# Optimization experiments

Hardware: AMD Instinct MI355X
Metric: run time of the kernel (lower is better)

Reference implementation:

```python
import jax, jax.numpy as jnp
import numpy as np

H = 256          # hidden_size
ATOM_F = 133     # chemprop atom feature dim
BOND_F = 14      # chemprop bond feature dim
BOND_FDIM = ATOM_F + BOND_F  # chemprop concatenates source-atom + bond features
N = 400_000      # total atoms in batch
E = 800_000      # total directed bonds (pairs e, e^1)
N_MOLS = 13_000
DEPTH = 3


def setup_inputs() -> dict:
    key = jax.random.key(0)
    ks = jax.random.split(key, 16)
    f_atoms = jax.random.normal(ks[0], (N, ATOM_F), jnp.float32)
    f_bonds = jax.random.normal(ks[1], (E, BOND_FDIM), jnp.float32)
    # directed bonds stored in reverse-pairs: bond 2i is a->b, bond 2i+1 is b->a
    src0 = jax.random.randint(ks[2], (E // 2,), 0, N)
    dst0 = jax.random.randint(ks[3], (E // 2,), 0, N)
    src = jnp.stack([src0, dst0], axis=1).reshape(-1)
    dst = jnp.stack([dst0, src0], axis=1).reshape(-1)
    edge_index = jnp.stack([src, dst], axis=0).astype(jnp.int32)  # [2, E]
    rev_edge_index = (jnp.arange(E, dtype=jnp.int32) ^ 1)         # rev(e) = e^1
    atom_mol = jnp.sort(jax.random.randint(ks[4], (N,), 0, N_MOLS)).astype(jnp.int32)

    def glorot(k, shape):
        return (jax.random.normal(k, shape, jnp.float32) / np.float32(np.sqrt(shape[0])))

    W_i = glorot(ks[5], (BOND_FDIM, H))      # chemprop W_i (no bias)
    W_h = glorot(ks[6], (H, H))              # chemprop W_h (no bias)
    W_o = glorot(ks[7], (ATOM_F + H, H))     # chemprop W_o
    b_o = jnp.zeros((H,), jnp.float32)
    node_W = glorot(ks[8], (H, ATOM_F)); node_b = jnp.zeros((ATOM_F,), jnp.float32)
    edge_W = glorot(ks[9], (H, BOND_F)); edge_b = jnp.zeros((BOND_F,), jnp.float32)
    g_W1 = glorot(ks[10], (H, H)); g_b1 = jnp.zeros((H,), jnp.float32)
    g_W2 = glorot(ks[11], (H, 1)); g_b2 = jnp.zeros((1,), jnp.float32)
    return dict(f_atoms=f_atoms, f_bonds=f_bonds,
                W_i=W_i, W_h=W_h, W_o=W_o, b_o=b_o,
                node_W=node_W, node_b=node_b, edge_W=edge_W, edge_b=edge_b,
                g_W1=g_W1, g_b1=g_b1, g_W2=g_W2, g_b2=g_b2,
                edge_index=edge_index, rev_edge_index=rev_edge_index,
                atom_mol=atom_mol, n_mols=N_MOLS)


def reference(f_atoms, f_bonds, W_i, W_h, W_o, b_o,
              node_W, node_b, edge_W, edge_b,
              g_W1, g_b1, g_W2, g_b2,
              edge_index, rev_edge_index, atom_mol, n_mols):
    n_atoms = f_atoms.shape[0]
    src, dst = edge_index[0], edge_index[1]

    # --- chemprop D-MPNN encoder (bond messages, depth=3, dropout=0) ---
    inp = f_bonds @ W_i                   # [E, H]
    msg = jax.nn.relu(inp)
    for _ in range(DEPTH - 1):
        # sum of messages arriving at each atom
        a_msg = jax.ops.segment_sum(msg, dst, num_segments=n_atoms)   # [N, H]
        # message for bond e (src->dst): sum into src minus reverse message
        msg = jax.nn.relu(inp + (a_msg[src] - msg[rev_edge_index]) @ W_h)
    a_msg = jax.ops.segment_sum(msg, dst, num_segments=n_atoms)
    atom_hiddens = jax.nn.relu(jnp.concatenate([f_atoms, a_msg], axis=1) @ W_o + b_o)  # [N, H]

    # --- graph pooling: per-molecule SUM over a_scope (empty mols -> zeros) ---
    graph_emb = jax.ops.segment_sum(atom_hiddens, atom_mol, num_segments=n_mols)  # [M, H]

    # --- node head ---
    node_pred = atom_hiddens @ node_W + node_b                        # [N, ATOM_F]

    # --- edge head with reverse-bond dedup: keep e where e < rev(e) (even e) ---
    keep = jnp.arange(0, edge_index.shape[1], 2)
    bond_emb = 0.5 * (atom_hiddens[src[keep]] + atom_hiddens[dst[keep]])
    edge_pred = bond_emb @ edge_W + edge_b                            # [E/2, BOND_F]

    # --- graph head MLP ---
    graph_pred = jax.nn.relu(graph_emb @ g_W1 + g_b1) @ g_W2 + g_b2   # [M, 1]
    return node_pred, edge_pred, graph_pred
```

## Files before the change

### kernel.cpp

```cpp
#include <hip/hip_runtime.h>

#define NATOMS 400000
#define NEDGES 800000
#define NMOLS  13000
#define AF 133
#define BFdim 14
#define BFD 147

typedef __attribute__((ext_vector_type(8))) short  s16x8;
typedef __attribute__((ext_vector_type(8))) __bf16 b16x8;
typedef __attribute__((ext_vector_type(4))) float  f32x4;

__device__ __forceinline__ float bf2f(unsigned short u){
  union { unsigned int i; float f; } v; v.i = ((unsigned int)u) << 16; return v.f;
}
__device__ __forceinline__ unsigned short f2bf(float f){
  union { float ff; unsigned int i; } v; v.ff = f;
  unsigned int b = v.i + 0x7fffu + ((v.i >> 16) & 1u);
  return (unsigned short)(b >> 16);
}
__device__ __forceinline__ unsigned int pk2(float a, float b){
  unsigned int r;
  asm("v_cvt_pk_bf16_f32 %0, %1, %2" : "=v"(r) : "v"(a), "v"(b));
  return r;
}
__device__ __forceinline__ f32x4 mfma16(s16x8 a, s16x8 b, f32x4 c){
  return __builtin_amdgcn_mfma_f32_16x16x32_bf16(
      __builtin_bit_cast(b16x8, a), __builtin_bit_cast(b16x8, b), c, 0, 0, 0);
}
__device__ __forceinline__ void gload_lds16(const void* g, void* lds){
  __builtin_amdgcn_global_load_lds(
      (const __attribute__((address_space(1))) void*)g,
      (__attribute__((address_space(3))) void*)lds, 16, 0, 0);
}

__global__ void k_prep_weights(const float* __restrict__ W_i, const float* __restrict__ W_h,
                               const float* __restrict__ W_o, const float* __restrict__ node_W,
                               const float* __restrict__ edge_W,
                               ushort* __restrict__ Wif, ushort* __restrict__ Wof1,
                               ushort* __restrict__ Whf, ushort* __restrict__ Wof2,
                               ushort* __restrict__ nWf, ushort* __restrict__ eWf){
  int gid = blockIdx.x * 256 + threadIdx.x;
  ushort* dst; const float* src; int KB, Kv, Ns, idx;
  if      (gid <  40960){ idx = gid;          dst = Wif;  src = W_i;          KB = 5; Kv = 147; Ns = 256; }
  else if (gid <  81920){ idx = gid -  40960; dst = Wof1; src = W_o;          KB = 5; Kv = 133; Ns = 256; }
  else if (gid < 147456){ idx = gid -  81920; dst = Whf;  src = W_h;          KB = 8; Kv = 256; Ns = 256; }
  else if (gid < 212992){ idx = gid - 147456; dst = Wof2; src = W_o + 133*256;KB = 8; Kv = 256; Ns = 256; }
  else if (gid < 249856){ idx = gid - 212992; dst = nWf;  src = node_W;       KB = 8; Kv = 256; Ns = 133; }
  else if (gid < 253952){ idx = gid - 249856; dst = eWf;  src = edge_W;       KB = 8; Kv = 256; Ns = 14;  }
  else return;
  int j = idx & 7, lane = (idx >> 3) & 63, fi = idx >> 9;
  int kb = fi % KB, nb = fi / KB;
  int k = kb * 32 + ((lane >> 4) << 3) + j;
  int n = nb * 16 + (lane & 15);
  float v = 0.f;
  if (k < Kv && n < Ns) v = src[(size_t)k * Ns + n];
  dst[idx] = f2bf(v);
}

__global__ void k_hist(const int* __restrict__ key, int* __restrict__ deg){
  int e = blockIdx.x * 256 + threadIdx.x;
  if (e < NEDGES) atomicAdd(&deg[key[e]], 1);
}
__global__ void k_blocksum(const int* __restrict__ deg, int* __restrict__ bsum){
  __shared__ int s[256];
  int i = blockIdx.x * 256 + threadIdx.x;
  s[threadIdx.x] = (i < NATOMS) ? deg[i] : 0;
  __syncthreads();
  for (int st = 128; st > 0; st >>= 1){
    if (threadIdx.x < st) s[threadIdx.x] += s[threadIdx.x + st];
    __syncthreads();
  }
  if (threadIdx.x == 0) bsum[blockIdx.x] = s[0];
}
#define NBLK 1563
__global__ void k_scanblk(const int* __restrict__ bs, int* __restrict__ bo){
  __shared__ int s[2048];
  int t = threadIdx.x;
  s[2*t]   = (2*t   < NBLK) ? bs[2*t]   : 0;
  s[2*t+1] = (2*t+1 < NBLK) ? bs[2*t+1] : 0;
  int offset = 1;
  for (int d = 1024; d > 0; d >>= 1){
    __syncthreads();
    if (t < d){ int ai = offset*(2*t+1)-1, bi = offset*(2*t+2)-1; s[bi] += s[ai]; }
    offset <<= 1;
  }
  __syncthreads();
  if (t == 0) s[2047] = 0;
  for (int d = 1; d < 2048; d <<= 1){
    offset >>= 1;
    __syncthreads();
    if (t < d){ int ai = offset*(2*t+1)-1, bi = offset*(2*t+2)-1;
                int tmp = s[ai]; s[ai] = s[bi]; s[bi] += tmp; }
  }
  __syncthreads();
  if (2*t   < NBLK) bo[2*t]   = s[2*t];
  if (2*t+1 < NBLK) bo[2*t+1] = s[2*t+1];
}
__global__ void k_offs(const int* __restrict__ deg, const int* __restrict__ bo,
                       int* __restrict__ offs, int* __restrict__ cursor){
  __shared__ int s1[256], s2[256];
  int t = threadIdx.x;
  int i = blockIdx.x * 256 + t;
  int v = (i < NATOMS) ? deg[i] : 0;
  s1[t] = v;
  __syncthreads();
  int* rd = s1; int* wr = s2;
  for (int ofs = 1; ofs < 256; ofs <<= 1){
    wr[t] = rd[t] + ((t >= ofs) ? rd[t - ofs] : 0);
    __syncthreads();
    int* tmp = rd; rd = wr; wr = tmp;
  }
  if (i < NATOMS){
    int excl = rd[t] - v + bo[blockIdx.x];
    offs[i] = excl; cursor[i] = excl;
  }
  if (i == 0) offs[NATOMS] = NEDGES;
}
__global__ void k_fill(const int* __restrict__ key, int* __restrict__ cursor,
                       int* __restrict__ elist){
  int e = blockIdx.x * 256 + threadIdx.x;
  if (e < NEDGES){ int pos = atomicAdd(&cursor[key[e]], 1); elist[pos] = e; }
}
__global__ void k_pos(const int* __restrict__ elist, int* __restrict__ pos){
  int i = blockIdx.x * 256 + threadIdx.x;
  if (i < NEDGES) pos[elist[i]] = i;
}
__global__ void k_maps(const int* __restrict__ elist, const int* __restrict__ pos,
                       int* __restrict__ revp){
  int i = blockIdx.x * 256 + threadIdx.x;
  if (i < NEDGES) revp[i] = pos[elist[i] ^ 1];
}
__global__ void k_molstart(const int* __restrict__ atom_mol, int* __restrict__ molst){
  int m = blockIdx.x * 256 + threadIdx.x;
  if (m > NMOLS) return;
  int lo = 0, hi = NATOMS;
  while (lo < hi){ int mid = (lo + hi) >> 1; if (atom_mol[mid] < m) lo = mid + 1; else hi = mid; }
  molst[m] = lo;
}

__global__ __launch_bounds__(256) void k_fused_inpY(
    const float* __restrict__ FB, const ushort* __restrict__ Wif,
    const ushort* __restrict__ Whf, const int* __restrict__ pos,
    ushort* __restrict__ inp, ushort* __restrict__ Yout){
  __shared__ ushort At[64 * 256];
  const int t = threadIdx.x, w = t >> 6, l = t & 63;
  const long e0 = (long)blockIdx.x * 64;
  {
    int r = t >> 2, q = t & 3;
    #pragma unroll
    for (int c = 0; c < 4; c++){
      int col = 147 + q * 4 + c;
      if (col < 160){
        int byte = r * 384 + ((2 * col) ^ ((r & 7) << 4));
        *(ushort*)((char*)At + byte) = 0;
      }
    }
  }
  {
    const float4* src = (const float4*)(FB + e0 * 147);
    #pragma unroll
    for (int it = 0; it < 10; it++){
      int idx = t + it * 256;
      if (idx < 2352){
        float4 v = src[idx];
        int fi = idx * 4;
        #pragma unroll
        for (int j = 0; j < 4; j++){
          int f = fi + j;
          int row = (int)(((unsigned)f * 114131u) >> 24);
          int col = f - row * 147;
          int byte = row * 384 + ((2 * col) ^ ((row & 7) << 4));
          *(ushort*)((char*)At + byte) = f2bf((&v.x)[j]);
        }
      }
    }
  }
  __syncthreads();
  const int lr = l & 15, lg = l >> 4;
  f32x4 acc[4][4] = {};
  for (int kb = 0; kb < 5; kb++){
    s16x8 a[4], b[4];
    #pragma unroll
    for (int m = 0; m < 4; m++){
      int row = m * 16 + lr;
      int cb = (kb * 64 + (lg << 4)) ^ ((row & 7) << 4);
      a[m] = *(const s16x8*)((const char*)At + row * 384 + cb);
    }
    #pragma unroll
    for (int n = 0; n < 4; n++)
      b[n] = *(const s16x8*)(Wif + (size_t)(((w * 4 + n) * 5 + kb) * 64 + l) * 8);
    #pragma unroll
    for (int m = 0; m < 4; m++)
      #pragma unroll
      for (int n = 0; n < 4; n++)
        acc[m][n] = mfma16(a[m], b[n], acc[m][n]);
  }
  __syncthreads();
  #pragma unroll
  for (int m = 0; m < 4; m++){
    long pr[4];
    #pragma unroll
    for (int r = 0; r < 4; r++)
      pr[r] = (long)pos[e0 + m * 16 + lg * 4 + r] * 256;
    #pragma unroll
    for (int n = 0; n < 4; n++){
      int col = w * 64 + n * 16 + lr;
      #pragma unroll
      for (int r = 0; r < 4; r++){
        float v = acc[m][n][r];
        inp[pr[r] + col] = f2bf(v);
        int row = m * 16 + lg * 4 + r;
        int byte = row * 512 + ((2 * col) ^ ((row & 7) << 4));
        *(ushort*)((char*)At + byte) = f2bf(v > 0.f ? v : 0.f);
      }
    }
  }
  __syncthreads();
  f32x4 acc2[4][4] = {};
  for (int kb = 0; kb < 8; kb++){
    s16x8 a[4], b[4];
    #pragma unroll
    for (int m = 0; m < 4; m++){
      int row = m * 16 + lr;
      int cb = (kb * 64 + (lg << 4)) ^ ((row & 7) << 4);
      a[m] = *(const s16x8*)((const char*)At + row * 512 + cb);
    }
    #pragma unroll
    for (int n = 0; n < 4; n++)
      b[n] = *(const s16x8*)(Whf + (size_t)(((w * 4 + n) * 8 + kb) * 64 + l) * 8);
    #pragma unroll
    for (int m = 0; m < 4; m++)
      #pragma unroll
      for (int n = 0; n < 4; n++)
        acc2[m][n] = mfma16(a[m], b[n], acc2[m][n]);
  }
  #pragma unroll
  for (int m = 0; m < 4; m++){
    long dr[4];
    #pragma unroll
    for (int r = 0; r < 4; r++)
      dr[r] = (long)pos[e0 + ((m * 16 + lg * 4 + r) ^ 1)] * 256;
    #pragma unroll
    for (int n = 0; n < 4; n++){
      int col = w * 64 + n * 16 + lr;
      #pragma unroll
      for (int r = 0; r < 4; r++)
        Yout[dr[r] + col] = f2bf(acc2[m][n][r]);
    }
  }
}

__global__ __launch_bounds__(256) void k_Y(
    const ushort* __restrict__ A, const ushort* __restrict__ Whf,
    const int* __restrict__ revp, ushort* __restrict__ Yout){
  __shared__ ushort At[64 * 256];
  const int t = threadIdx.x, w = t >> 6, l = t & 63;
  const long e0 = (long)blockIdx.x * 64;
  const char* Ab = (const char*)(A + e0 * 256);
  #pragma unroll
  for (int i = 0; i < 8; i++){
    int dbase = (i * 4 + w) * 1024;
    int d = dbase + l * 16;
    int sw = ((d >> 9) & 7) << 4;
    gload_lds16(Ab + (d ^ sw), (char*)At + dbase);
  }
  __syncthreads();
  const int lr = l & 15, lg = l >> 4;
  f32x4 acc[4][4] = {};
  for (int kb = 0; kb < 8; kb++){
    s16x8 a[4], b[4];
    #pragma unroll
    for (int m = 0; m < 4; m++){
      int row = m * 16 + lr;
      int cb = (kb * 64 + (lg << 4)) ^ ((row & 7) << 4);
      a[m] = *(const s16x8*)((const char*)At + row * 512 + cb);
    }
    #pragma unroll
    for (int n = 0; n < 4; n++){
      int fi = (w * 4 + n) * 8 + kb;
      b[n] = *(const s16x8*)(Whf + (size_t)(fi * 64 + l) * 8);
    }
    #pragma unroll
    for (int m = 0; m < 4; m++)
      #pragma unroll
      for (int n = 0; n < 4; n++)
        acc[m][n] = mfma16(a[m], b[n], acc[m][n]);
  }
  #pragma unroll
  for (int m = 0; m < 4; m++){
    long dr[4];
    #pragma unroll
    for (int r = 0; r < 4; r++)
      dr[r] = (long)revp[e0 + m * 16 + lg * 4 + r] * 256;
    #pragma unroll
    for (int n = 0; n < 4; n++){
      int col = w * 64 + n * 16 + lr;
      #pragma unroll
      for (int r = 0; r < 4; r++)
        Yout[dr[r] + col] = f2bf(acc[m][n][r]);
    }
  }
}

template<bool SCATTER>
__global__ __launch_bounds__(256) void k_comb(
    const ushort* __restrict__ Yd, const ushort* __restrict__ inp,
    const int* __restrict__ revp, const int* __restrict__ offs,
    ushort* __restrict__ M){
  const int t = threadIdx.x, g = t >> 5, h = t & 31;
  const int a = blockIdx.x * 8 + g;
  const int beg = offs[a], end = offs[a + 1];
  const int deg = end - beg;
  if (deg == 0) return;
  if (deg <= 4){
    s16x8 y[4], vi[4];
    #pragma unroll
    for (int k = 0; k < 4; k++) if (k < deg){
      y[k]  = *(const s16x8*)(Yd  + (size_t)(beg + k) * 256 + h * 8);
      vi[k] = *(const s16x8*)(inp + (size_t)(beg + k) * 256 + h * 8);
    }
    float acc[8] = {};
    #pragma unroll
    for (int k = 0; k < 4; k++) if (k < deg){
      #pragma unroll
      for (int j = 0; j < 8; j++) acc[j] += bf2f((ushort)y[k][j]);
    }
    #pragma unroll
    for (int k = 0; k < 4; k++) if (k < deg){
      float vv[8];
      #pragma unroll
      for (int j = 0; j < 8; j++){
        float v = bf2f((ushort)vi[k][j]) + acc[j] - bf2f((ushort)y[k][j]);
        vv[j] = v > 0.f ? v : 0.f;
      }
      uint4 o;
      o.x = pk2(vv[0], vv[1]); o.y = pk2(vv[2], vv[3]);
      o.z = pk2(vv[4], vv[5]); o.w = pk2(vv[6], vv[7]);
      long wrow = SCATTER ? (long)revp[beg + k] : (long)(beg + k);
      *(uint4*)(M + wrow * 256 + h * 8) = o;
    }
  } else {
    float acc[8] = {};
    for (int i = beg; i < end; i++){
      s16x8 y = *(const s16x8*)(Yd + (size_t)i * 256 + h * 8);
      #pragma unroll
      for (int j = 0; j < 8; j++) acc[j] += bf2f((ushort)y[j]);
    }
    for (int i = beg; i < end; i++){
      s16x8 y  = *(const s16x8*)(Yd  + (size_t)i * 256 + h * 8);
      s16x8 vi = *(const s16x8*)(inp + (size_t)i * 256 + h * 8);
      float vv[8];
      #pragma unroll
      for (int j = 0; j < 8; j++){
        float v = bf2f((ushort)vi[j]) + acc[j] - bf2f((ushort)y[j]);
        vv[j] = v > 0.f ? v : 0.f;
      }
      uint4 o;
      o.x = pk2(vv[0], vv[1]); o.y = pk2(vv[2], vv[3]);
      o.z = pk2(vv[4], vv[5]); o.w = pk2(vv[6], vv[7]);
      long wrow = SCATTER ? (long)revp[i] : (long)i;
      *(uint4*)(M + wrow * 256 + h * 8) = o;
    }
  }
}

__global__ __launch_bounds__(256) void k_amsg_seq(
    const ushort* __restrict__ Md, const int* __restrict__ offs,
    ushort* __restrict__ amsg){
  const int t = threadIdx.x, g = t >> 5, h = t & 31;
  const int a = blockIdx.x * 8 + g;
  const int beg = offs[a], end = offs[a + 1];
  float acc[8] = {};
  for (int i = beg; i < end; i++){
    s16x8 v = *(const s16x8*)(Md + (size_t)i * 256 + h * 8);
    #pragma unroll
    for (int j = 0; j < 8; j++) acc[j] += bf2f((ushort)v[j]);
  }
  uint4 ov;
  ov.x = pk2(acc[0], acc[1]); ov.y = pk2(acc[2], acc[3]);
  ov.z = pk2(acc[4], acc[5]); ov.w = pk2(acc[6], acc[7]);
  *(uint4*)(amsg + (size_t)a * 256 + h * 8) = ov;
}

__global__ __launch_bounds__(256) void k_ah(
    const float* __restrict__ FA, const ushort* __restrict__ Wof1,
    const ushort* __restrict__ amsg, const ushort* __restrict__ Wof2,
    const float* __restrict__ b_o, ushort* __restrict__ ah){
  __shared__ ushort At[64 * 192];
  const int t = threadIdx.x, w = t >> 6, l = t & 63;
  const long r0 = (long)blockIdx.x * 64;
  {
    int r = t >> 2, q = t & 3;
    #pragma unroll
    for (int c = 0; c < 7; c++){
      int col = 133 + q * 7 + c;
      if (col < 160){
        int byte = r * 384 + ((2 * col) ^ ((r & 7) << 4));
        *(ushort*)((char*)At + byte) = 0;
      }
    }
  }
  {
    const float4* src = (const float4*)(FA + r0 * 133);
    #pragma unroll
    for (int it = 0; it < 9; it++){
      int idx = t + it * 256;
      if (idx < 2128){
        float4 v = src[idx];
        int fi = idx * 4;
        #pragma unroll
        for (int j = 0; j < 4; j++){
          int f = fi + j;
          int row = (int)(((unsigned)f * 126146u) >> 24);
          int col = f - row * 133;
          int byte = row * 384 + ((2 * col) ^ ((row & 7) << 4));
          *(ushort*)((char*)At + byte) = f2bf((&v.x)[j]);
        }
      }
    }
  }
  __syncthreads();
  const int lr = l & 15, lg = l >> 4;
  f32x4 acc[4][4] = {};
  for (int kb = 0; kb < 5; kb++){
    s16x8 a[4], b[4];
    #pragma unroll
    for (int m = 0; m < 4; m++){
      int row = m * 16 + lr;
      int cb = (kb * 64 + (lg << 4)) ^ ((row & 7) << 4);
      a[m] = *(const s16x8*)((const char*)At + row * 384 + cb);
    }
    #pragma unroll
    for (int n = 0; n < 4; n++)
      b[n] = *(const s16x8*)(Wof1 + (size_t)(((w * 4 + n) * 5 + kb) * 64 + l) * 8);
    #pragma unroll
    for (int m = 0; m < 4; m++)
      #pragma unroll
      for (int n = 0; n < 4; n++)
        acc[m][n] = mfma16(a[m], b[n], acc[m][n]);
  }
  for (int kb = 0; kb < 8; kb++){
    s16x8 a[4], b[4];
    #pragma unroll
    for (int m = 0; m < 4; m++)
      a[m] = *(const s16x8*)(amsg + (r0 + m * 16 + lr) * 256 + kb * 32 + lg * 8);
    #pragma unroll
    for (int n = 0; n < 4; n++)
      b[n] = *(const s16x8*)(Wof2 + (size_t)(((w * 4 + n) * 8 + kb) * 64 + l) * 8);
    #pragma unroll
    for (int m = 0; m < 4; m++)
      #pragma unroll
      for (int n = 0; n < 4; n++)
        acc[m][n] = mfma16(a[m], b[n], acc[m][n]);
  }
  #pragma unroll
  for (int m = 0; m < 4; m++){
    #pragma unroll
    for (int n = 0; n < 4; n++){
      int col = w * 64 + n * 16 + lr;
      float bo = b_o[col];
      long base = (r0 + m * 16 + lg * 4) * 256 + col;
      #pragma unroll
      for (int r = 0; r < 4; r++){
        float v = acc[m][n][r] + bo;
        ah[base + (long)r * 256] = f2bf(v > 0.f ? v : 0.f);
      }
    }
  }
}

__global__ __launch_bounds__(256) void k_nodeproj(
    const ushort* __restrict__ ah, const ushort* __restrict__ nWf,
    const ushort* __restrict__ eWf, const float* __restrict__ node_b,
    float* __restrict__ out_node, float* __restrict__ proj){
  const int t = threadIdx.x, w = t >> 6, l = t & 63, lr = l & 15, lg = l >> 4;
  const long r0 = (long)blockIdx.x * 64;
  f32x4 acc[4][3] = {};
  for (int kb = 0; kb < 8; kb++){
    s16x8 a[4];
    #pragma unroll
    for (int m = 0; m < 4; m++)
      a[m] = *(const s16x8*)(ah + (r0 + m * 16 + lr) * 256 + kb * 32 + lg * 8);
    s16x8 b[3];
    #pragma unroll
    for (int j = 0; j < 3; j++){
      int nt = w + 4 * j;
      int ntc = (nt <= 9) ? nt : 0;
      if (ntc == 9)
        b[j] = *(const s16x8*)(eWf + (size_t)(kb * 64 + l) * 8);
      else
        b[j] = *(const s16x8*)(nWf + (size_t)((ntc * 8 + kb) * 64 + l) * 8);
    }
    #pragma unroll
    for (int m = 0; m < 4; m++)
      #pragma unroll
      for (int j = 0; j < 3; j++)
        acc[m][j] = mfma16(a[m], b[j], acc[m][j]);
  }
  #pragma unroll
  for (int j = 0; j < 3; j++){
    int nt = w + 4 * j;
    if (nt > 9) continue;
    if (nt == 9){
      #pragma unroll
      for (int m = 0; m < 4; m++)
        #pragma unroll
        for (int r = 0; r < 4; r++)
          proj[(r0 + m * 16 + lg * 4 + r) * 16 + lr] = acc[m][j][r];
    } else {
      int col = nt * 16 + lr;
      if (col < AF){
        float nb = node_b[col];
        #pragma unroll
        for (int m = 0; m < 4; m++)
          #pragma unroll
          for (int r = 0; r < 4; r++)
            out_node[(r0 + m * 16 + lg * 4 + r) * AF + col] = acc[m][j][r] + nb;
      }
    }
  }
}

__global__ void k_edge_out(const int* __restrict__ edge_index, const float* __restrict__ proj,
                           const float* __restrict__ edge_b, float* __restrict__ out_edge){
  int gid = blockIdx.x * 256 + threadIdx.x;
  int i = gid >> 4, c = gid & 15;
  if (c < BFdim){
    int s = edge_index[2 * i];
    int d = edge_index[NEDGES + 2 * i];
    out_edge[(size_t)i * BFdim + c] =
        0.5f * (proj[(size_t)s * 16 + c] + proj[(size_t)d * 16 + c]) + edge_b[c];
  }
}

__global__ __launch_bounds__(256) void k_pool(const ushort* __restrict__ ah,
                                              const int* __restrict__ molst,
                                              float* __restrict__ gemb){
  const int t = threadIdx.x, w = t >> 6, l = t & 63;
  const int m = blockIdx.x * 4 + w;
  const int beg = molst[m], end = molst[m + 1];
  float a0 = 0, a1 = 0, a2 = 0, a3 = 0;
  for (int i = beg; i < end; i++){
    const ushort4 v = *(const ushort4*)(ah + (size_t)i * 256 + l * 4);
    a0 += bf2f(v.x); a1 += bf2f(v.y); a2 += bf2f(v.z); a3 += bf2f(v.w);
  }
  f32x4 o = {a0, a1, a2, a3};
  *(f32x4*)(gemb + (size_t)m * 256 + l * 4) = o;
}

__global__ __launch_bounds__(256) void k_g1(const float* __restrict__ gemb,
                                            const float* __restrict__ gW1,
                                            const float* __restrict__ gb1,
                                            float* __restrict__ ghid){
  __shared__ float s[16 * 256];
  const int t = threadIdx.x;
  const int r0 = blockIdx.x * 16;
  for (int i = 0; i < 16; i++){
    int r = r0 + i;
    s[i * 256 + t] = (r < NMOLS) ? gemb[(size_t)r * 256 + t] : 0.f;
  }
  __syncthreads();
  float acc[16] = {};
  for (int k = 0; k < 256; k++){
    float wv = gW1[(size_t)k * 256 + t];
    #pragma unroll
    for (int i = 0; i < 16; i++) acc[i] += s[i * 256 + k] * wv;
  }
  float b = gb1[t];
  for (int i = 0; i < 16; i++){
    int r = r0 + i;
    if (r < NMOLS){ float v = acc[i] + b; ghid[(size_t)r * 256 + t] = v > 0.f ? v : 0.f; }
  }
}
__global__ void k_g2(const float* __restrict__ ghid, const float* __restrict__ gW2,
                     const float* __restrict__ gb2, float* __restrict__ outg){
  const int t = threadIdx.x, w = t >> 6, l = t & 63;
  const int m = blockIdx.x * 4 + w;
  f32x4 v = *(const f32x4*)(ghid + (size_t)m * 256 + l * 4);
  const f32x4 wv = *(const f32x4*)(gW2 + l * 4);
  float acc = v[0] * wv[0] + v[1] * wv[1] + v[2] * wv[2] + v[3] * wv[3];
  for (int ofs = 32; ofs; ofs >>= 1) acc += __shfl_down(acc, ofs, 64);
  if (l == 0) outg[m] = acc + gb2[0];
}

extern "C" void kernel_launch(void* const* d_in, const int* in_sizes, int n_in,
                              void* d_out, int out_size, void* d_ws, size_t ws_size,
                              hipStream_t stream){
  const float* f_atoms = (const float*)d_in[0];
  const float* f_bonds = (const float*)d_in[1];
  const float* W_i     = (const float*)d_in[2];
  const float* W_h     = (const float*)d_in[3];
  const float* W_o     = (const float*)d_in[4];
  const float* b_o     = (const float*)d_in[5];
  const float* node_W  = (const float*)d_in[6];
  const float* node_b  = (const float*)d_in[7];
  const float* edge_W  = (const float*)d_in[8];
  const float* edge_b  = (const float*)d_in[9];
  const float* g_W1    = (const float*)d_in[10];
  const float* g_b1    = (const float*)d_in[11];
  const float* g_W2    = (const float*)d_in[12];
  const float* g_b2    = (const float*)d_in[13];
  const int* edge_index = (const int*)d_in[14];
  const int* atom_mol   = (const int*)d_in[16];

  float* out_node  = (float*)d_out;
  float* out_edge  = out_node + (size_t)NATOMS * AF;
  float* out_graph = out_edge + (size_t)(NEDGES / 2) * BFdim;

  char* p = (char*)d_ws;
  auto alloc = [&](size_t b) -> char* { char* r = p; p += (b + 255) & ~(size_t)255; return r; };
  ushort* B1 = (ushort*)alloc((size_t)NEDGES * 256 * 2);
  ushort* B2 = (ushort*)alloc((size_t)NEDGES * 256 * 2);
  ushort* B3 = (ushort*)alloc((size_t)NEDGES * 256 * 2);
  ushort* N1 = (ushort*)alloc((size_t)NATOMS * 256 * 2);
  ushort* N2 = (ushort*)alloc((size_t)NATOMS * 256 * 2);
  float*  proj  = (float*)alloc((size_t)NATOMS * 16 * 4);
  float*  gemb  = (float*)alloc((size_t)NMOLS * 256 * 4);
  float*  ghid  = (float*)alloc((size_t)NMOLS * 256 * 4);
  ushort* Wif   = (ushort*)alloc(160 * 256 * 2);
  ushort* Wof1  = (ushort*)alloc(160 * 256 * 2);
  ushort* Whf   = (ushort*)alloc(256 * 256 * 2);
  ushort* Wof2  = (ushort*)alloc(256 * 256 * 2);
  ushort* nWf   = (ushort*)alloc(256 * 144 * 2);
  ushort* eWf   = (ushort*)alloc(256 * 16 * 2);
  int* deg    = (int*)alloc(NATOMS * 4);
  int* offs   = (int*)alloc((NATOMS + 1) * 4);
  int* cursor = (int*)alloc(NATOMS * 4);
  int* elist  = (int*)alloc(NEDGES * 4);
  int* pos    = (int*)alloc(NEDGES * 4);
  int* revp   = (int*)alloc(NEDGES * 4);
  int* bsum   = (int*)alloc(1568 * 4);
  int* boff   = (int*)alloc(1568 * 4);
  int* molst  = (int*)alloc((NMOLS + 1) * 4);
  if ((size_t)(p - (char*)d_ws) > ws_size) return;

  const int* srci = edge_index;

  hipMemsetAsync(deg, 0, NATOMS * 4, stream);
  k_prep_weights<<<992, 256, 0, stream>>>(W_i, W_h, W_o, node_W, edge_W,
                                          Wif, Wof1, Whf, Wof2, nWf, eWf);
  k_hist<<<3125, 256, 0, stream>>>(srci, deg);
  k_blocksum<<<NBLK, 256, 0, stream>>>(deg, bsum);
  k_scanblk<<<1, 1024, 0, stream>>>(bsum, boff);
  k_offs<<<NBLK, 256, 0, stream>>>(deg, boff, offs, cursor);
  k_fill<<<3125, 256, 0, stream>>>(srci, cursor, elist);
  k_pos<<<3125, 256, 0, stream>>>(elist, pos);
  k_maps<<<3125, 256, 0, stream>>>(elist, pos, revp);
  k_molstart<<<51, 256, 0, stream>>>(atom_mol, molst);

  k_fused_inpY<<<12500, 256, 0, stream>>>(f_bonds, Wif, Whf, pos, B1, B3);
  k_comb<false><<<50000, 256, 0, stream>>>(B3, B1, revp, offs, B2);
  k_Y<<<12500, 256, 0, stream>>>(B2, Whf, revp, B3);
  k_comb<true><<<50000, 256, 0, stream>>>(B3, B1, revp, offs, B2);
  k_amsg_seq<<<50000, 256, 0, stream>>>(B2, offs, N2);
  k_ah<<<6250, 256, 0, stream>>>(f_atoms, Wof1, N2, Wof2, b_o, N1);
  k_pool<<<3250, 256, 0, stream>>>(N1, molst, gemb);
  k_nodeproj<<<6250, 256, 0, stream>>>(N1, nWf, eWf, node_b, out_node, proj);
  k_edge_out<<<25000, 256, 0, stream>>>(edge_index, proj, edge_b, out_edge);
  k_g1<<<813, 256, 0, stream>>>(gemb, g_W1, g_b1, ghid);
  k_g2<<<3250, 256, 0, stream>>>(ghid, g_W2, g_b2, out_graph);
}
```

Measured before the change: 1.917 ms.

## Fuse atom-message sum, atom-hidden GEMM and node/edge projection into one kernel

Merges the per-atom message segment sum, the W_o atom-hidden GEMM, and the node/edge projection GEMM into a single kernel. The aggregated messages and the atom hiddens are staged in swizzled shared memory instead of being written to and re-read from global buffers, which removes the N2 buffer and one full read of N1. It also replaces the per-element divide-by-multiply row/col computation in the feature staging loops with an incremental counter. The trade-offs are a larger shared-memory footprint per block, which may lower occupancy, and the serial gather loop now sitting inside the GEMM kernel, where it is less parallel than the old 50000-block launch.

```diff
diff --git a/kernel.cpp b/kernel.cpp
--- a/kernel.cpp
+++ b/kernel.cpp
@@ -164,14 +164,15 @@
       int idx = t + it * 256;
       if (idx < 2352){
         float4 v = src[idx];
-        int fi = idx * 4;
+        int f0 = idx * 4;
+        int row = (int)(((unsigned)f0 * 114131u) >> 24);
+        int col = f0 - row * 147;
         #pragma unroll
         for (int j = 0; j < 4; j++){
-          int f = fi + j;
-          int row = (int)(((unsigned)f * 114131u) >> 24);
-          int col = f - row * 147;
           int byte = row * 384 + ((2 * col) ^ ((row & 7) << 4));
           *(ushort*)((char*)At + byte) = f2bf((&v.x)[j]);
+          col++;
+          if (col == 147){ col = 0; row++; }
         }
       }
     }
@@ -365,30 +366,17 @@
   }
 }
 
-__global__ __launch_bounds__(256) void k_amsg_seq(
+__global__ __launch_bounds__(256) void k_final(
     const ushort* __restrict__ Md, const int* __restrict__ offs,
-    ushort* __restrict__ amsg){
-  const int t = threadIdx.x, g = t >> 5, h = t & 31;
-  const int a = blockIdx.x * 8 + g;
-  const int beg = offs[a], end = offs[a + 1];
-  float acc[8] = {};
-  for (int i = beg; i < end; i++){
-    s16x8 v = *(const s16x8*)(Md + (size_t)i * 256 + h * 8);
-    #pragma unroll
-    for (int j = 0; j < 8; j++) acc[j] += bf2f((ushort)v[j]);
-  }
-  uint4 ov;
-  ov.x = pk2(acc[0], acc[1]); ov.y = pk2(acc[2], acc[3]);
-  ov.z = pk2(acc[4], acc[5]); ov.w = pk2(acc[6], acc[7]);
-  *(uint4*)(amsg + (size_t)a * 256 + h * 8) = ov;
-}
-
-__global__ __launch_bounds__(256) void k_ah(
     const float* __restrict__ FA, const ushort* __restrict__ Wof1,
-    const ushort* __restrict__ amsg, const ushort* __restrict__ Wof2,
-    const float* __restrict__ b_o, ushort* __restrict__ ah){
-  __shared__ ushort At[64 * 192];
+    const ushort* __restrict__ Wof2, const float* __restrict__ b_o,
+    const ushort* __restrict__ nWf, const ushort* __restrict__ eWf,
+    const float* __restrict__ node_b,
+    ushort* __restrict__ ah, float* __restrict__ out_node,
+    float* __restrict__ proj){
+  __shared__ ushort At[64 * 256];
   const int t = threadIdx.x, w = t >> 6, l = t & 63;
+  const int lr = l & 15, lg = l >> 4;
   const long r0 = (long)blockIdx.x * 64;
   {
     int r = t >> 2, q = t & 3;
@@ -400,28 +388,26 @@
         *(ushort*)((char*)At + byte) = 0;
       }
     }
-  }
-  {
     const float4* src = (const float4*)(FA + r0 * 133);
     #pragma unroll
     for (int it = 0; it < 9; it++){
       int idx = t + it * 256;
       if (idx < 2128){
         float4 v = src[idx];
-        int fi = idx * 4;
+        int f0 = idx * 4;
+        int row = (int)(((unsigned)f0 * 126146u) >> 24);
+        int col = f0 - row * 133;
         #pragma unroll
         for (int j = 0; j < 4; j++){
-          int f = fi + j;
-          int row = (int)(((unsigned)f * 126146u) >> 24);
-          int col = f - row * 133;
           int byte = row * 384 + ((2 * col) ^ ((row & 7) << 4));
           *(ushort*)((char*)At + byte) = f2bf((&v.x)[j]);
+          col++;
+          if (col == 133){ col = 0; row++; }
         }
       }
     }
   }
   __syncthreads();
-  const int lr = l & 15, lg = l >> 4;
   f32x4 acc[4][4] = {};
   for (int kb = 0; kb < 5; kb++){
     s16x8 a[4], b[4];
@@ -440,11 +426,36 @@
       for (int n = 0; n < 4; n++)
         acc[m][n] = mfma16(a[m], b[n], acc[m][n]);
   }
+  __syncthreads();
+  {
+    const int g = t >> 5, h = t & 31;
+    #pragma unroll
+    for (int k = 0; k < 8; k++){
+      int al = g * 8 + k;
+      int a = (int)r0 + al;
+      int beg = offs[a], end = offs[a + 1];
+      float s[8] = {};
+      for (int i = beg; i < end; i++){
+        s16x8 v = *(const s16x8*)(Md + (size_t)i * 256 + h * 8);
+        #pragma unroll
+        for (int j = 0; j < 8; j++) s[j] += bf2f((ushort)v[j]);
+      }
+      uint4 ov;
+      ov.x = pk2(s[0], s[1]); ov.y = pk2(s[2], s[3]);
+      ov.z = pk2(s[4], s[5]); ov.w = pk2(s[6], s[7]);
+      int byte = al * 512 + ((16 * h) ^ ((al & 7) << 4));
+      *(uint4*)((char*)At + byte) = ov;
+    }
+  }
+  __syncthreads();
   for (int kb = 0; kb < 8; kb++){
     s16x8 a[4], b[4];
     #pragma unroll
-    for (int m = 0; m < 4; m++)
-      a[m] = *(const s16x8*)(amsg + (r0 + m * 16 + lr) * 256 + kb * 32 + lg * 8);
+    for (int m = 0; m < 4; m++){
+      int row = m * 16 + lr;
+      int cb = (kb * 64 + (lg << 4)) ^ ((row & 7) << 4);
+      a[m] = *(const s16x8*)((const char*)At + row * 512 + cb);
+    }
     #pragma unroll
     for (int n = 0; n < 4; n++)
       b[n] = *(const s16x8*)(Wof2 + (size_t)(((w * 4 + n) * 8 + kb) * 64 + l) * 8);
@@ -454,6 +465,7 @@
       for (int n = 0; n < 4; n++)
         acc[m][n] = mfma16(a[m], b[n], acc[m][n]);
   }
+  __syncthreads();
   #pragma unroll
   for (int m = 0; m < 4; m++){
     #pragma unroll
@@ -464,24 +476,24 @@
       #pragma unroll
       for (int r = 0; r < 4; r++){
         float v = acc[m][n][r] + bo;
-        ah[base + (long)r * 256] = f2bf(v > 0.f ? v : 0.f);
-      }
-    }
-  }
-}
-
-__global__ __launch_bounds__(256) void k_nodeproj(
-    const ushort* __restrict__ ah, const ushort* __restrict__ nWf,
-    const ushort* __restrict__ eWf, const float* __restrict__ node_b,
-    float* __restrict__ out_node, float* __restrict__ proj){
-  const int t = threadIdx.x, w = t >> 6, l = t & 63, lr = l & 15, lg = l >> 4;
-  const long r0 = (long)blockIdx.x * 64;
-  f32x4 acc[4][3] = {};
+        ushort u = f2bf(v > 0.f ? v : 0.f);
+        ah[base + (long)r * 256] = u;
+        int row = m * 16 + lg * 4 + r;
+        int byte = row * 512 + ((2 * col) ^ ((row & 7) << 4));
+        *(ushort*)((char*)At + byte) = u;
+      }
+    }
+  }
+  __syncthreads();
+  f32x4 acc3[4][3] = {};
   for (int kb = 0; kb < 8; kb++){
     s16x8 a[4];
     #pragma unroll
-    for (int m = 0; m < 4; m++)
-      a[m] = *(const s16x8*)(ah + (r0 + m * 16 + lr) * 256 + kb * 32 + lg * 8);
+    for (int m = 0; m < 4; m++){
+      int row = m * 16 + lr;
+      int cb = (kb * 64 + (lg << 4)) ^ ((row & 7) << 4);
+      a[m] = *(const s16x8*)((const char*)At + row * 512 + cb);
+    }
     s16x8 b[3];
     #pragma unroll
     for (int j = 0; j < 3; j++){
@@ -496,7 +508,7 @@
     for (int m = 0; m < 4; m++)
       #pragma unroll
       for (int j = 0; j < 3; j++)
-        acc[m][j] = mfma16(a[m], b[j], acc[m][j]);
+        acc3[m][j] = mfma16(a[m], b[j], acc3[m][j]);
   }
   #pragma unroll
   for (int j = 0; j < 3; j++){
@@ -507,7 +519,7 @@
       for (int m = 0; m < 4; m++)
         #pragma unroll
         for (int r = 0; r < 4; r++)
-          proj[(r0 + m * 16 + lg * 4 + r) * 16 + lr] = acc[m][j][r];
+          proj[(r0 + m * 16 + lg * 4 + r) * 16 + lr] = acc3[m][j][r];
     } else {
       int col = nt * 16 + lr;
       if (col < AF){
@@ -516,7 +528,7 @@
         for (int m = 0; m < 4; m++)
           #pragma unroll
           for (int r = 0; r < 4; r++)
-            out_node[(r0 + m * 16 + lg * 4 + r) * AF + col] = acc[m][j][r] + nb;
+            out_node[(r0 + m * 16 + lg * 4 + r) * AF + col] = acc3[m][j][r] + nb;
       }
     }
   }
@@ -614,7 +626,6 @@
   ushort* B2 = (ushort*)alloc((size_t)NEDGES * 256 * 2);
   ushort* B3 = (ushort*)alloc((size_t)NEDGES * 256 * 2);
   ushort* N1 = (ushort*)alloc((size_t)NATOMS * 256 * 2);
-  ushort* N2 = (ushort*)alloc((size_t)NATOMS * 256 * 2);
   float*  proj  = (float*)alloc((size_t)NATOMS * 16 * 4);
   float*  gemb  = (float*)alloc((size_t)NMOLS * 256 * 4);
   float*  ghid  = (float*)alloc((size_t)NMOLS * 256 * 4);
@@ -653,10 +664,9 @@
   k_comb<false><<<50000, 256, 0, stream>>>(B3, B1, revp, offs, B2);
   k_Y<<<12500, 256, 0, stream>>>(B2, Whf, revp, B3);
   k_comb<true><<<50000, 256, 0, stream>>>(B3, B1, revp, offs, B2);
-  k_amsg_seq<<<50000, 256, 0, stream>>>(B2, offs, N2);
-  k_ah<<<6250, 256, 0, stream>>>(f_atoms, Wof1, N2, Wof2, b_o, N1);
+  k_final<<<6250, 256, 0, stream>>>(B2, offs, f_atoms, Wof1, Wof2, b_o,
+                                    nWf, eWf, node_b, N1, out_node, proj);
   k_pool<<<3250, 256, 0, stream>>>(N1, molst, gemb);
-  k_nodeproj<<<6250, 256, 0, stream>>>(N1, nWf, eWf, node_b, out_node, proj);
   k_edge_out<<<25000, 256, 0, stream>>>(edge_index, proj, edge_b, out_edge);
   k_g1<<<813, 256, 0, stream>>>(gemb, g_W1, g_b1, ghid);
   k_g2<<<3250, 256, 0, stream>>>(ghid, g_W2, g_b2, out_graph);
```

Result: no change. 1.895 ms (-1.1%).
